# Optimization experiments

Measured on AMD Instinct MI355X. Metric: run time of the kernel, lower is better.

## Reference

```python
import jax, jax.numpy as jnp
import numpy as np

N = 500000
EMB = 256
CONT = {0: [0, 1, 4, 6, 7, 8, 9, 10, 11, 12, 13],
        1: [0, 1, 4, 5, 6, 7, 8, 9, 10, 11, 12, 13],
        2: [1, 2, 4, 5, 6, 7, 8, 9, 10, 11, 12, 13],
        3: [2, 3, 4, 5, 6, 7, 8, 9, 10, 11, 12, 13]}
DISC = {0: [2, 3, 5], 1: [2, 3], 2: [0], 3: [0, 1]}
DIMS = {0: {2: 96, 3: 8, 5: 2}, 1: {2: 4, 3: 22}, 2: {0: 6}, 3: {0: 15, 1: 96}}


def _splits(n):
    # emb_dim split across n discrete features, remainder to the first ones
    per, r = EMB // n, EMB % n
    return [per + (1 if i < r else 0) for i in range(n)]


def setup_inputs() -> dict:
    key = jax.random.key(0)
    x = jax.random.normal(jax.random.fold_in(key, 0), (N, 14), jnp.float32)
    # discrete columns must hold valid integer codes for every node type using them
    col_max = {0: 6, 1: 96, 2: 4, 3: 8, 5: 2}
    for c, m in col_max.items():
        v = jax.random.randint(jax.random.fold_in(key, 100 + c), (N,), 0, m)
        x = x.at[:, c].set(v.astype(jnp.float32))
    node_types = jax.random.randint(jax.random.fold_in(key, 1), (N,), 0, 4)
    inp = {"x": x, "node_types": node_types}
    for t in range(4):
        fan_in = len(CONT[t])
        s = float(np.sqrt(6.0 / (fan_in + EMB)))  # xavier_uniform bound
        inp[f"W{t}"] = jax.random.uniform(jax.random.fold_in(key, 10 + t), (EMB, fan_in), jnp.float32, -s, s)
        inp[f"b{t}"] = jax.random.uniform(jax.random.fold_in(key, 20 + t), (EMB,), jnp.float32, -0.05, 0.05)
        dims = _splits(len(DISC[t]))
        for i, c in enumerate(DISC[t]):
            vocab = DIMS[t][c]
            se = float(np.sqrt(6.0 / (vocab + dims[i])))
            inp[f"E{t}_{c}"] = jax.random.uniform(jax.random.fold_in(key, 1000 + 10 * t + c), (vocab, dims[i]), jnp.float32, -se, se)
    return inp


def _forward(x, node_types, Ws, bs, Es):
    out = jnp.zeros((x.shape[0], EMB), x.dtype)
    for t in range(4):  # fixed small set of node types (static MoE dispatch)
        mask = node_types == t  # [N]
        # discrete embeddings: gather per feature column, concat to [N, EMB]
        disc = jnp.concatenate(
            [Es[t][i][x[:, c].astype(jnp.int32)] for i, c in enumerate(DISC[t])], axis=1)
        # continuous projection: [N, in_dim] @ [in_dim, EMB] + bias
        cont = x[:, jnp.array(CONT[t])] @ Ws[t].T + bs[t]
        out = jnp.where(mask[:, None], disc + cont, out)
    return out


def reference(x, node_types, W0, b0, W1, b1, W2, b2, W3, b3,
              E0_2, E0_3, E0_5, E1_2, E1_3, E2_0, E3_0, E3_1):
    Ws = [W0, W1, W2, W3]
    bs = [b0, b1, b2, b3]
    Es = {0: [E0_2, E0_3, E0_5], 1: [E1_2, E1_3], 2: [E2_0], 3: [E3_0, E3_1]}
    return _forward(x, node_types, Ws, bs, Es)
```

## Files before the change

### kernel.cpp

```cpp
#include <hip/hip_runtime.h>

typedef float fvec4 __attribute__((ext_vector_type(4)));

#define NBLK 256
#define TPB  1024
#define CN   512

#define LAUNDER_PTR(p) asm volatile("" : "+v"(p))

#define O_E0_2 0
#define O_E0_3 8256
#define O_E0_5 8936
#define O_E1_2 9108
#define O_E1_3 9620
#define O_E2_0 12436
#define O_E3_0 13972
#define O_E3_1 15892
#define NTAB   28180
#define XSH    NTAB
#define IDX    (XSH + CN * 16)
#define CNTO   (IDX + 4 * CN)
#define SMEM_FLOATS (CNTO + 4)
#define SMEM_BYTES  (SMEM_FLOATS * 4)

extern __shared__ float smem[];

#define TYPE_BLOCK(T, NW, WPTR, BPTR, SC, ST, PB, ...)                         \
  {                                                                            \
    const int m = cnt_ro[T];                                                   \
    const float* Wp = WPTR; LAUNDER_PTR(Wp);                                   \
    const float* bp = BPTR; LAUNDER_PTR(bp);                                   \
    float w[NW];                                                               \
    _Pragma("unroll")                                                          \
    for (int k = 0; k < NW; ++k) w[k] = Wp[e * NW + k];                        \
    const float bias = bp[e];                                                  \
    for (int g = h; g < m; g += 4) {                                           \
      const int nl = idx_ro[T * CN + g];                                       \
      const float* xr = &smem[XSH + nl * 16];                                  \
      const float4 ra = *reinterpret_cast<const float4*>(xr);                  \
      const float4 rb = *reinterpret_cast<const float4*>(xr + 4);              \
      const float4 rc = *reinterpret_cast<const float4*>(xr + 8);              \
      const float2 rd = *reinterpret_cast<const float2*>(xr + 12);             \
      const int code = (int)xr[SC];                                            \
      const float emb = smem[(PB) + code * (ST)];                              \
      float acc = bias;                                                        \
      __VA_ARGS__                                                              \
      out[(cb + nl) * 256 + e] = acc + emb;                                    \
    }                                                                          \
  }

__global__ __launch_bounds__(TPB, 1)
void node_enc_kernel(const float* __restrict__ x,
                     const int* __restrict__ node_types,
                     const float* __restrict__ W0, const float* __restrict__ b0,
                     const float* __restrict__ E0_2, const float* __restrict__ E0_3,
                     const float* __restrict__ E0_5,
                     const float* __restrict__ W1, const float* __restrict__ b1,
                     const float* __restrict__ E1_2, const float* __restrict__ E1_3,
                     const float* __restrict__ W2, const float* __restrict__ b2,
                     const float* __restrict__ E2_0,
                     const float* __restrict__ W3, const float* __restrict__ b3,
                     const float* __restrict__ E3_0, const float* __restrict__ E3_1,
                     float* __restrict__ out, int n_nodes)
{
    const int tid = threadIdx.x;
    const int e   = tid & 255;
    const int h   = tid >> 8;

    auto copy_tab = [&](const float* __restrict__ src, int dst, int n) {
        if ((((uintptr_t)src) & 15) == 0) {
            const int nv = n >> 2;
            for (int i = tid; i < nv; i += TPB) {
                const fvec4 v = *(reinterpret_cast<const fvec4*>(src) + i);
                *reinterpret_cast<fvec4*>(&smem[dst + (i << 2)]) = v;
            }
            for (int i = (nv << 2) + tid; i < n; i += TPB) smem[dst + i] = src[i];
        } else {
            for (int i = tid; i < n; i += TPB) smem[dst + i] = src[i];
        }
    };
    copy_tab(E0_2, O_E0_2, 8256);
    copy_tab(E0_3, O_E0_3, 680);
    copy_tab(E0_5, O_E0_5, 170);
    copy_tab(E1_2, O_E1_2, 512);
    copy_tab(E1_3, O_E1_3, 2816);
    copy_tab(E2_0, O_E2_0, 1536);
    copy_tab(E3_0, O_E3_0, 1920);
    copy_tab(E3_1, O_E3_1, 12288);

    int sc0, st0, pb0;
    if (e < 86)       { sc0 = 2; st0 = 86; pb0 = O_E0_2 + e; }
    else if (e < 171) { sc0 = 3; st0 = 85; pb0 = O_E0_3 + (e - 86); }
    else              { sc0 = 5; st0 = 85; pb0 = O_E0_5 + (e - 171); }
    int sc1, st1, pb1;
    if (e < 128) { sc1 = 2; st1 = 128; pb1 = O_E1_2 + e; }
    else         { sc1 = 3; st1 = 128; pb1 = O_E1_3 + (e - 128); }
    const int sc2 = 0, st2 = 256, pb2 = O_E2_0 + e;
    int sc3, st3, pb3;
    if (e < 128) { sc3 = 0; st3 = 128; pb3 = O_E3_0 + e; }
    else         { sc3 = 1; st3 = 128; pb3 = O_E3_1 + (e - 128); }

    const int nch = (n_nodes + CN - 1) / CN;
    const int c0  = (int)(((long long)blockIdx.x * nch) / NBLK);
    const int c1  = (int)(((long long)(blockIdx.x + 1) * nch) / NBLK);

    int* const idx_m = reinterpret_cast<int*>(&smem[IDX]);
    int* const cnt_m = reinterpret_cast<int*>(&smem[CNTO]);
    const int* idx_ro = idx_m;
    const int* cnt_ro = cnt_m;

    auto stage_issue = [&](int c, fvec4& r0, fvec4& r1,
                           float& rs, int& ty, int& nv, int& total, int& cnn) {
        const long long cb = (long long)c * CN;
        cnn   = min(CN, (int)(n_nodes - cb));
        total = cnn * 14;
        nv    = total >> 2;
        const fvec4* vsrc = reinterpret_cast<const fvec4*>(x + cb * 14);
        if (tid < nv)          r0 = __builtin_nontemporal_load(vsrc + tid);
        if (tid + TPB < nv)    r1 = __builtin_nontemporal_load(vsrc + tid + TPB);
        const int sf = (nv << 2) + tid;
        if (sf < total) rs = x[cb * 14 + sf];
        if (tid < cnn)  ty = node_types[cb + tid];
    };
    auto stage_write = [&](const fvec4& r0, const fvec4& r1,
                           float rs, int nv, int total) {
        auto wr1 = [&](int i, const fvec4& v) {
            const int f = i << 2;
            int node = f / 14, col = f - node * 14;
            #pragma unroll
            for (int j = 0; j < 4; ++j) {
                smem[XSH + node * 16 + col] = v[j];
                if (++col == 14) { col = 0; ++node; }
            }
        };
        if (tid < nv)        wr1(tid, r0);
        if (tid + TPB < nv)  wr1(tid + TPB, r1);
        const int sf = (nv << 2) + tid;
        if (sf < total) { const int node = sf / 14, col = sf - node * 14; smem[XSH + node * 16 + col] = rs; }
    };

    auto do_chunk = [&](int c) {
        const long long cb = (long long)c * CN;
        TYPE_BLOCK(0, 11, W0, b0, sc0, st0, pb0,
            acc = fmaf(w[0],  ra.x, acc);
            acc = fmaf(w[1],  ra.y, acc);
            acc = fmaf(w[2],  rb.x, acc);
            acc = fmaf(w[3],  rb.z, acc);
            acc = fmaf(w[4],  rb.w, acc);
            acc = fmaf(w[5],  rc.x, acc);
            acc = fmaf(w[6],  rc.y, acc);
            acc = fmaf(w[7],  rc.z, acc);
            acc = fmaf(w[8],  rc.w, acc);
            acc = fmaf(w[9],  rd.x, acc);
            acc = fmaf(w[10], rd.y, acc);)
        TYPE_BLOCK(1, 12, W1, b1, sc1, st1, pb1,
            acc = fmaf(w[0],  ra.x, acc);
            acc = fmaf(w[1],  ra.y, acc);
            acc = fmaf(w[2],  rb.x, acc);
            acc = fmaf(w[3],  rb.y, acc);
            acc = fmaf(w[4],  rb.z, acc);
            acc = fmaf(w[5],  rb.w, acc);
            acc = fmaf(w[6],  rc.x, acc);
            acc = fmaf(w[7],  rc.y, acc);
            acc = fmaf(w[8],  rc.z, acc);
            acc = fmaf(w[9],  rc.w, acc);
            acc = fmaf(w[10], rd.x, acc);
            acc = fmaf(w[11], rd.y, acc);)
        TYPE_BLOCK(2, 12, W2, b2, sc2, st2, pb2,
            acc = fmaf(w[0],  ra.y, acc);
            acc = fmaf(w[1],  ra.z, acc);
            acc = fmaf(w[2],  rb.x, acc);
            acc = fmaf(w[3],  rb.y, acc);
            acc = fmaf(w[4],  rb.z, acc);
            acc = fmaf(w[5],  rb.w, acc);
            acc = fmaf(w[6],  rc.x, acc);
            acc = fmaf(w[7],  rc.y, acc);
            acc = fmaf(w[8],  rc.z, acc);
            acc = fmaf(w[9],  rc.w, acc);
            acc = fmaf(w[10], rd.x, acc);
            acc = fmaf(w[11], rd.y, acc);)
        TYPE_BLOCK(3, 12, W3, b3, sc3, st3, pb3,
            acc = fmaf(w[0],  ra.z, acc);
            acc = fmaf(w[1],  ra.w, acc);
            acc = fmaf(w[2],  rb.x, acc);
            acc = fmaf(w[3],  rb.y, acc);
            acc = fmaf(w[4],  rb.z, acc);
            acc = fmaf(w[5],  rb.w, acc);
            acc = fmaf(w[6],  rc.x, acc);
            acc = fmaf(w[7],  rc.y, acc);
            acc = fmaf(w[8],  rc.z, acc);
            acc = fmaf(w[9],  rc.w, acc);
            acc = fmaf(w[10], rd.x, acc);
            acc = fmaf(w[11], rd.y, acc);)
    };

    {
        fvec4 r0, r1; float rs = 0.f; int ty = 0, nv = 0, total = 0, cnn = 0;
        if (c0 < c1) {
            stage_issue(c0, r0, r1, rs, ty, nv, total, cnn);
            stage_write(r0, r1, rs, nv, total);
            if (tid < 4) cnt_m[tid] = 0;
        }
        __syncthreads();
        if (c0 < c1 && tid < cnn) {
            const int p = atomicAdd(&cnt_m[ty], 1);
            idx_m[ty * CN + p] = tid;
        }
        __syncthreads();
    }

    for (int c = c0; c < c1; ++c) {
        fvec4 r0, r1; float rs = 0.f; int ty = 0, nv = 0, total = 0, cnn = 0;
        const bool hasnext = (c + 1 < c1);
        if (hasnext) stage_issue(c + 1, r0, r1, rs, ty, nv, total, cnn);
        do_chunk(c);
        __syncthreads();
        if (hasnext) {
            stage_write(r0, r1, rs, nv, total);
            if (tid < 4) cnt_m[tid] = 0;
        }
        __syncthreads();
        if (hasnext && tid < cnn) {
            const int p = atomicAdd(&cnt_m[ty], 1);
            idx_m[ty * CN + p] = tid;
        }
        __syncthreads();
    }
}

extern "C" void kernel_launch(void* const* d_in, const int* in_sizes, int n_in,
                              void* d_out, int out_size, void* d_ws, size_t ws_size,
                              hipStream_t stream) {
    const float* xp   = (const float*)d_in[0];
    const int*   ntp  = (const int*)d_in[1];
    const float* W0 = (const float*)d_in[2];
    const float* b0 = (const float*)d_in[3];
    const float* E0_2 = (const float*)d_in[4];
    const float* E0_3 = (const float*)d_in[5];
    const float* E0_5 = (const float*)d_in[6];
    const float* W1 = (const float*)d_in[7];
    const float* b1 = (const float*)d_in[8];
    const float* E1_2 = (const float*)d_in[9];
    const float* E1_3 = (const float*)d_in[10];
    const float* W2 = (const float*)d_in[11];
    const float* b2 = (const float*)d_in[12];
    const float* E2_0 = (const float*)d_in[13];
    const float* W3 = (const float*)d_in[14];
    const float* b3 = (const float*)d_in[15];
    const float* E3_0 = (const float*)d_in[16];
    const float* E3_1 = (const float*)d_in[17];
    float* outp = (float*)d_out;

    const int n_nodes = in_sizes[1];

    hipFuncSetAttribute(reinterpret_cast<const void*>(node_enc_kernel),
                        hipFuncAttributeMaxDynamicSharedMemorySize, SMEM_BYTES);

    node_enc_kernel<<<NBLK, TPB, SMEM_BYTES, stream>>>(
        xp, ntp, W0, b0, E0_2, E0_3, E0_5, W1, b1, E1_2, E1_3,
        W2, b2, E2_0, W3, b3, E3_0, E3_1, outp, n_nodes);
}
```

Before: 156.0 us.

## Compute four output columns per thread with float4 stores

Each thread now owns four consecutive embedding columns (64 threads per node row, 16 node groups) instead of one column (256 threads per row, 4 groups). The x row loaded from LDS is reused across four columns and the output is written as a 128-bit store, which cuts LDS traffic and store instruction count. In exchange each thread holds 4x the weight registers (up to 48 floats plus per-column descriptors), which raises register pressure at 1024 threads per block, and the embedding lookups become four scattered LDS reads per node.

Result: faster. 133.3 us (-14.5%).

```diff
diff --git a/kernel.cpp b/kernel.cpp
--- a/kernel.cpp
+++ b/kernel.cpp
@@ -4,6 +4,7 @@
 
 #define NBLK 256
 #define TPB  1024
+#define NG   16
 #define CN   512
 
 #define LAUNDER_PTR(p) asm volatile("" : "+v"(p))
@@ -25,27 +26,46 @@
 
 extern __shared__ float smem[];
 
-#define TYPE_BLOCK(T, NW, WPTR, BPTR, SC, ST, PB, ...)                         \
+#define FMA4(K, XV)                                   \
+    acc.x = fmaf(w[0][K], (XV), acc.x);               \
+    acc.y = fmaf(w[1][K], (XV), acc.y);               \
+    acc.z = fmaf(w[2][K], (XV), acc.z);               \
+    acc.w = fmaf(w[3][K], (XV), acc.w);
+
+#define TYPE_BLOCK(T, NW, WPTR, BPTR, DESC_STMT, FMA_LIST)                     \
   {                                                                            \
     const int m = cnt_ro[T];                                                   \
     const float* Wp = WPTR; LAUNDER_PTR(Wp);                                   \
     const float* bp = BPTR; LAUNDER_PTR(bp);                                   \
-    float w[NW];                                                               \
+    float w[4][NW];                                                            \
     _Pragma("unroll")                                                          \
-    for (int k = 0; k < NW; ++k) w[k] = Wp[e * NW + k];                        \
-    const float bias = bp[e];                                                  \
-    for (int g = h; g < m; g += 4) {                                           \
+    for (int j = 0; j < 4; ++j) {                                              \
+      _Pragma("unroll")                                                        \
+      for (int k = 0; k < NW; ++k) w[j][k] = Wp[(4 * q + j) * NW + k];         \
+    }                                                                          \
+    float4 bias;                                                               \
+    bias.x = bp[4 * q]; bias.y = bp[4 * q + 1];                                \
+    bias.z = bp[4 * q + 2]; bias.w = bp[4 * q + 3];                            \
+    int sc[4], st[4], pb[4];                                                   \
+    _Pragma("unroll")                                                          \
+    for (int j = 0; j < 4; ++j) { const int col = 4 * q + j; DESC_STMT }       \
+    for (int g = h; g < m; g += NG) {                                          \
       const int nl = idx_ro[T * CN + g];                                       \
       const float* xr = &smem[XSH + nl * 16];                                  \
       const float4 ra = *reinterpret_cast<const float4*>(xr);                  \
       const float4 rb = *reinterpret_cast<const float4*>(xr + 4);              \
       const float4 rc = *reinterpret_cast<const float4*>(xr + 8);              \
       const float2 rd = *reinterpret_cast<const float2*>(xr + 12);             \
-      const int code = (int)xr[SC];                                            \
-      const float emb = smem[(PB) + code * (ST)];                              \
-      float acc = bias;                                                        \
-      __VA_ARGS__                                                              \
-      out[(cb + nl) * 256 + e] = acc + emb;                                    \
+      float4 acc = bias;                                                       \
+      FMA_LIST                                                                 \
+      float ev[4];                                                             \
+      _Pragma("unroll")                                                        \
+      for (int j = 0; j < 4; ++j) {                                            \
+        const int code = (int)xr[sc[j]];                                       \
+        ev[j] = smem[pb[j] + code * st[j]];                                    \
+      }                                                                        \
+      acc.x += ev[0]; acc.y += ev[1]; acc.z += ev[2]; acc.w += ev[3];          \
+      *reinterpret_cast<float4*>(&out[(cb + nl) * 256 + 4 * q]) = acc;         \
     }                                                                          \
   }
 
@@ -64,8 +84,8 @@
                      float* __restrict__ out, int n_nodes)
 {
     const int tid = threadIdx.x;
-    const int e   = tid & 255;
-    const int h   = tid >> 8;
+    const int q   = tid & 63;
+    const int h   = tid >> 6;
 
     auto copy_tab = [&](const float* __restrict__ src, int dst, int n) {
         if ((((uintptr_t)src) & 15) == 0) {
@@ -87,18 +107,6 @@
     copy_tab(E2_0, O_E2_0, 1536);
     copy_tab(E3_0, O_E3_0, 1920);
     copy_tab(E3_1, O_E3_1, 12288);
-
-    int sc0, st0, pb0;
-    if (e < 86)       { sc0 = 2; st0 = 86; pb0 = O_E0_2 + e; }
-    else if (e < 171) { sc0 = 3; st0 = 85; pb0 = O_E0_3 + (e - 86); }
-    else              { sc0 = 5; st0 = 85; pb0 = O_E0_5 + (e - 171); }
-    int sc1, st1, pb1;
-    if (e < 128) { sc1 = 2; st1 = 128; pb1 = O_E1_2 + e; }
-    else         { sc1 = 3; st1 = 128; pb1 = O_E1_3 + (e - 128); }
-    const int sc2 = 0, st2 = 256, pb2 = O_E2_0 + e;
-    int sc3, st3, pb3;
-    if (e < 128) { sc3 = 0; st3 = 128; pb3 = O_E3_0 + e; }
-    else         { sc3 = 1; st3 = 128; pb3 = O_E3_1 + (e - 128); }
 
     const int nch = (n_nodes + CN - 1) / CN;
     const int c0  = (int)(((long long)blockIdx.x * nch) / NBLK);
@@ -141,57 +149,30 @@
 
     auto do_chunk = [&](int c) {
         const long long cb = (long long)c * CN;
-        TYPE_BLOCK(0, 11, W0, b0, sc0, st0, pb0,
-            acc = fmaf(w[0],  ra.x, acc);
-            acc = fmaf(w[1],  ra.y, acc);
-            acc = fmaf(w[2],  rb.x, acc);
-            acc = fmaf(w[3],  rb.z, acc);
-            acc = fmaf(w[4],  rb.w, acc);
-            acc = fmaf(w[5],  rc.x, acc);
-            acc = fmaf(w[6],  rc.y, acc);
-            acc = fmaf(w[7],  rc.z, acc);
-            acc = fmaf(w[8],  rc.w, acc);
-            acc = fmaf(w[9],  rd.x, acc);
-            acc = fmaf(w[10], rd.y, acc);)
-        TYPE_BLOCK(1, 12, W1, b1, sc1, st1, pb1,
-            acc = fmaf(w[0],  ra.x, acc);
-            acc = fmaf(w[1],  ra.y, acc);
-            acc = fmaf(w[2],  rb.x, acc);
-            acc = fmaf(w[3],  rb.y, acc);
-            acc = fmaf(w[4],  rb.z, acc);
-            acc = fmaf(w[5],  rb.w, acc);
-            acc = fmaf(w[6],  rc.x, acc);
-            acc = fmaf(w[7],  rc.y, acc);
-            acc = fmaf(w[8],  rc.z, acc);
-            acc = fmaf(w[9],  rc.w, acc);
-            acc = fmaf(w[10], rd.x, acc);
-            acc = fmaf(w[11], rd.y, acc);)
-        TYPE_BLOCK(2, 12, W2, b2, sc2, st2, pb2,
-            acc = fmaf(w[0],  ra.y, acc);
-            acc = fmaf(w[1],  ra.z, acc);
-            acc = fmaf(w[2],  rb.x, acc);
-            acc = fmaf(w[3],  rb.y, acc);
-            acc = fmaf(w[4],  rb.z, acc);
-            acc = fmaf(w[5],  rb.w, acc);
-            acc = fmaf(w[6],  rc.x, acc);
-            acc = fmaf(w[7],  rc.y, acc);
-            acc = fmaf(w[8],  rc.z, acc);
-            acc = fmaf(w[9],  rc.w, acc);
-            acc = fmaf(w[10], rd.x, acc);
-            acc = fmaf(w[11], rd.y, acc);)
-        TYPE_BLOCK(3, 12, W3, b3, sc3, st3, pb3,
-            acc = fmaf(w[0],  ra.z, acc);
-            acc = fmaf(w[1],  ra.w, acc);
-            acc = fmaf(w[2],  rb.x, acc);
-            acc = fmaf(w[3],  rb.y, acc);
-            acc = fmaf(w[4],  rb.z, acc);
-            acc = fmaf(w[5],  rb.w, acc);
-            acc = fmaf(w[6],  rc.x, acc);
-            acc = fmaf(w[7],  rc.y, acc);
-            acc = fmaf(w[8],  rc.z, acc);
-            acc = fmaf(w[9],  rc.w, acc);
-            acc = fmaf(w[10], rd.x, acc);
-            acc = fmaf(w[11], rd.y, acc);)
+        TYPE_BLOCK(0, 11, W0, b0,
+            if (col < 86)       { sc[j] = 2; st[j] = 86; pb[j] = O_E0_2 + col; }
+            else if (col < 171) { sc[j] = 3; st[j] = 85; pb[j] = O_E0_3 + col - 86; }
+            else                { sc[j] = 5; st[j] = 85; pb[j] = O_E0_5 + col - 171; },
+            FMA4(0,  ra.x) FMA4(1,  ra.y) FMA4(2,  rb.x) FMA4(3,  rb.z)
+            FMA4(4,  rb.w) FMA4(5,  rc.x) FMA4(6,  rc.y) FMA4(7,  rc.z)
+            FMA4(8,  rc.w) FMA4(9,  rd.x) FMA4(10, rd.y))
+        TYPE_BLOCK(1, 12, W1, b1,
+            if (col < 128) { sc[j] = 2; st[j] = 128; pb[j] = O_E1_2 + col; }
+            else           { sc[j] = 3; st[j] = 128; pb[j] = O_E1_3 + col - 128; },
+            FMA4(0,  ra.x) FMA4(1,  ra.y) FMA4(2,  rb.x) FMA4(3,  rb.y)
+            FMA4(4,  rb.z) FMA4(5,  rb.w) FMA4(6,  rc.x) FMA4(7,  rc.y)
+            FMA4(8,  rc.z) FMA4(9,  rc.w) FMA4(10, rd.x) FMA4(11, rd.y))
+        TYPE_BLOCK(2, 12, W2, b2,
+            sc[j] = 0; st[j] = 256; pb[j] = O_E2_0 + col;,
+            FMA4(0,  ra.y) FMA4(1,  ra.z) FMA4(2,  rb.x) FMA4(3,  rb.y)
+            FMA4(4,  rb.z) FMA4(5,  rb.w) FMA4(6,  rc.x) FMA4(7,  rc.y)
+            FMA4(8,  rc.z) FMA4(9,  rc.w) FMA4(10, rd.x) FMA4(11, rd.y))
+        TYPE_BLOCK(3, 12, W3, b3,
+            if (col < 128) { sc[j] = 0; st[j] = 128; pb[j] = O_E3_0 + col; }
+            else           { sc[j] = 1; st[j] = 128; pb[j] = O_E3_1 + col - 128; },
+            FMA4(0,  ra.z) FMA4(1,  ra.w) FMA4(2,  rb.x) FMA4(3,  rb.y)
+            FMA4(4,  rb.z) FMA4(5,  rb.w) FMA4(6,  rc.x) FMA4(7,  rc.y)
+            FMA4(8,  rc.z) FMA4(9,  rc.w) FMA4(10, rd.x) FMA4(11, rd.y))
     };
 
     {
```
